# Kernel tuning notes

Measured on AMD Instinct MI355X. Metric: run time of the kernel, lower is better.

Reference implementation:

```python
import jax, jax.numpy as jnp
import numpy as np

N = 50000      # nodes
E = 800000     # edges (avg degree 16)
IN = 128       # in_channels
HID = 32       # hidden_channels per head
HEADS = 4
OUT = 64       # out_channels (last layer, heads=1, concat=False)
ED = 32        # edge_dim
NEG_SLOPE = 0.2


def _gatv2_layer(x, src, dst, ea, Wl, bl, Wr, br, We, att, bias, concat):
    """PyG GATv2Conv: lin_l -> source (x_j), lin_r -> target (x_i),
    score = att . leaky_relu(x_i + x_j + lin_edge(edge_attr)), segment-softmax over dst,
    out = scatter_add(alpha * x_j) per head, then concat or mean heads, plus bias."""
    n = x.shape[0]
    H, C = att.shape
    xl = (x @ Wl + bl).reshape(-1, H, C)   # [N,H,C] source transform
    xr = (x @ Wr + br).reshape(-1, H, C)   # [N,H,C] target transform
    ee = (ea @ We).reshape(-1, H, C)       # [E,H,C] edge transform
    m = jax.nn.leaky_relu(xl[src] + xr[dst] + ee, NEG_SLOPE)  # [E,H,C]
    a = jnp.einsum('ehc,hc->eh', m, att)   # [E,H] attention logits
    amax = jax.ops.segment_max(a, dst, num_segments=n)        # [N,H]
    ex = jnp.exp(a - amax[dst])
    den = jax.ops.segment_sum(ex, dst, num_segments=n)        # [N,H]
    alpha = ex / (den[dst] + 1e-16)        # [E,H] segment softmax
    out = jax.ops.segment_sum(xl[src] * alpha[..., None], dst, num_segments=n)  # [N,H,C]
    out = out.reshape(n, H * C) if concat else out.mean(axis=1)
    return out + bias


def setup_inputs() -> dict:
    key = jax.random.key(0)
    ks = jax.random.split(key, 20)
    s = 0.05
    HC = HEADS * HID
    inp = {
        'x': jax.random.normal(ks[0], (N, IN), jnp.float32),
        'edge_index': jax.random.randint(ks[1], (2, E), 0, N, jnp.int32),
        'edge_attr': jax.random.normal(ks[2], (E, ED), jnp.float32),
        # layer 1: GATv2Conv(IN -> HID, heads=HEADS, concat=True, edge_dim=ED)
        'Wl1': jax.random.normal(ks[3], (IN, HC), jnp.float32) * s,
        'bl1': jnp.zeros((HC,), jnp.float32),
        'Wr1': jax.random.normal(ks[4], (IN, HC), jnp.float32) * s,
        'br1': jnp.zeros((HC,), jnp.float32),
        'We1': jax.random.normal(ks[5], (ED, HC), jnp.float32) * s,
        'att1': jax.random.normal(ks[6], (HEADS, HID), jnp.float32) * s,
        'bias1': jnp.zeros((HC,), jnp.float32),
        # layer 2: GATv2Conv(HC -> OUT, heads=1, concat=False, edge_dim=ED)
        'Wl2': jax.random.normal(ks[7], (HC, OUT), jnp.float32) * s,
        'bl2': jnp.zeros((OUT,), jnp.float32),
        'Wr2': jax.random.normal(ks[8], (HC, OUT), jnp.float32) * s,
        'br2': jnp.zeros((OUT,), jnp.float32),
        'We2': jax.random.normal(ks[9], (ED, OUT), jnp.float32) * s,
        'att2': jax.random.normal(ks[10], (1, OUT), jnp.float32) * s,
        'bias2': jnp.zeros((OUT,), jnp.float32),
    }
    return inp


def reference(x, edge_index, edge_attr, Wl1, bl1, Wr1, br1, We1, att1, bias1,
              Wl2, bl2, Wr2, br2, We2, att2, bias2):
    src, dst = edge_index[0], edge_index[1]
    h = _gatv2_layer(x, src, dst, edge_attr, Wl1, bl1, Wr1, br1, We1, att1, bias1, concat=True)
    h = jax.nn.elu(h)
    out = _gatv2_layer(h, src, dst, edge_attr, Wl2, bl2, Wr2, br2, We2, att2, bias2, concat=False)
    return out
```

## Files before the change

kernel.cpp:

```cpp
#include <hip/hip_runtime.h>
#include <stdint.h>

#define N_NODES 50000
#define N_EDGES 800000

struct Ptrs { const void* p[16]; int n[16]; };

typedef __attribute__((ext_vector_type(8))) short bf16x8;
typedef __attribute__((ext_vector_type(4))) float f32x4;

__device__ __forceinline__ float bf2f(unsigned short u){
  union { unsigned int i; float f; } v; v.i = ((unsigned int)u) << 16; return v.f;
}
__device__ __forceinline__ float lo16(unsigned int u){ union { unsigned int i; float f; } v; v.i = u << 16; return v.f; }
__device__ __forceinline__ float hi16(unsigned int u){ union { unsigned int i; float f; } v; v.i = u & 0xffff0000u; return v.f; }
__device__ __forceinline__ unsigned short f2bf(float f){
  if (!(f == f)) return 0;
  unsigned int x = __float_as_uint(f);
  unsigned int r = (x + 0x7fffu + ((x >> 16) & 1u)) >> 16;
  return (unsigned short)r;
}
__device__ __forceinline__ float fin(float v){
  if (!(v == v)) return 0.f;
  return fminf(fmaxf(v, -1e30f), 1e30f);
}
__device__ __forceinline__ float loadF(const void* p, int f32, size_t idx){
  return f32 ? ((const float*)p)[idx] : bf2f(((const unsigned short*)p)[idx]);
}

__device__ __forceinline__ void stageW(unsigned short* dst, const void* src, int n, int f32, int tid){
  if (f32) {
    for (int i = tid * 8; i < n; i += 2048) {
      float4 a = *(const float4*)((const float*)src + i);
      float4 b = *(const float4*)((const float*)src + i + 4);
      uint4 u;
      u.x = (unsigned)f2bf(a.x) | ((unsigned)f2bf(a.y) << 16);
      u.y = (unsigned)f2bf(a.z) | ((unsigned)f2bf(a.w) << 16);
      u.z = (unsigned)f2bf(b.x) | ((unsigned)f2bf(b.y) << 16);
      u.w = (unsigned)f2bf(b.z) | ((unsigned)f2bf(b.w) << 16);
      *(uint4*)(dst + i) = u;
    }
  } else {
    for (int i = tid * 8; i < n; i += 2048)
      *(uint4*)(dst + i) = *(const uint4*)((const unsigned short*)src + i);
  }
}

__global__ __launch_bounds__(256) void k_detect(Ptrs tl, int* __restrict__ flags)
{
  __shared__ int red[256];
  int b = blockIdx.x, t = threadIdx.x;
  const unsigned short* p = (const unsigned short*)tl.p[b];
  int n = tl.n[b]; if (n > 16384) n = 16384;
  int crazy = 0;
  for (int i = t; i < n; i += 256) {
    unsigned short u = p[i];
    if (u) {
      int ex = (u >> 7) & 0xFF;
      if (ex == 0xFF || ex < 0x60) crazy++;
    }
  }
  red[t] = crazy; __syncthreads();
  for (int off = 128; off; off >>= 1) { if (t < off) red[t] += red[t + off]; __syncthreads(); }
  if (t == 0) flags[b] = (red[0] * 10 > n) ? 1 : 0;
}

__global__ __launch_bounds__(256) void k_zero(int* __restrict__ p, int n)
{
  int i = blockIdx.x * 256 + threadIdx.x;
  if (i < n) p[i] = 0;
}

__global__ __launch_bounds__(256) void k_gemm1(
    const void* __restrict__ x,
    const void* __restrict__ Wl, const void* __restrict__ bl,
    const void* __restrict__ Wr, const void* __restrict__ br,
    const int* __restrict__ flags,
    unsigned int* __restrict__ xlp, unsigned int* __restrict__ xrp)
{
  __shared__ float xs[32 * 132];
  __shared__ unsigned short ws[128 * 128];
  const void* W  = blockIdx.y ? Wr : Wl;
  const void* bb = blockIdx.y ? br : bl;
  int fW = blockIdx.y ? flags[4] : flags[2];
  int fB = blockIdx.y ? flags[5] : flags[3];
  int fX = flags[0];
  unsigned int* outp = blockIdx.y ? xrp : xlp;
  int tid = threadIdx.x;
  int row0 = blockIdx.x * 32;
  stageW(ws, W, 128 * 128, fW, tid);
  for (int i = tid * 4; i < 32 * 128; i += 1024) {
    int r = i >> 7, k = i & 127;
    int row = row0 + r;
    float4 v = make_float4(0.f, 0.f, 0.f, 0.f);
    if (row < N_NODES) {
      if (fX) v = *(const float4*)((const float*)x + (size_t)row * 128 + k);
      else {
        uint2 u = *(const uint2*)((const unsigned short*)x + (size_t)row * 128 + k);
        v.x = lo16(u.x); v.y = hi16(u.x); v.z = lo16(u.y); v.w = hi16(u.y);
      }
    }
    *(float4*)(xs + r * 132 + k) = v;
  }
  __syncthreads();
  int r = tid >> 3, cg = tid & 7;
  float acc[16];
#pragma unroll
  for (int j = 0; j < 16; j++) acc[j] = 0.f;
#pragma unroll 4
  for (int k = 0; k < 128; k++) {
    float xv = xs[r * 132 + k];
    uint4 p0 = *(const uint4*)(ws + k * 128 + cg * 8);
    uint4 p1 = *(const uint4*)(ws + k * 128 + 64 + cg * 8);
    acc[0]  = fmaf(xv, lo16(p0.x), acc[0]);  acc[1]  = fmaf(xv, hi16(p0.x), acc[1]);
    acc[2]  = fmaf(xv, lo16(p0.y), acc[2]);  acc[3]  = fmaf(xv, hi16(p0.y), acc[3]);
    acc[4]  = fmaf(xv, lo16(p0.z), acc[4]);  acc[5]  = fmaf(xv, hi16(p0.z), acc[5]);
    acc[6]  = fmaf(xv, lo16(p0.w), acc[6]);  acc[7]  = fmaf(xv, hi16(p0.w), acc[7]);
    acc[8]  = fmaf(xv, lo16(p1.x), acc[8]);  acc[9]  = fmaf(xv, hi16(p1.x), acc[9]);
    acc[10] = fmaf(xv, lo16(p1.y), acc[10]); acc[11] = fmaf(xv, hi16(p1.y), acc[11]);
    acc[12] = fmaf(xv, lo16(p1.z), acc[12]); acc[13] = fmaf(xv, hi16(p1.z), acc[13]);
    acc[14] = fmaf(xv, lo16(p1.w), acc[14]); acc[15] = fmaf(xv, hi16(p1.w), acc[15]);
  }
  int row = row0 + r;
  if (row < N_NODES) {
    unsigned int* op = outp + (size_t)row * 64;
    int tt = cg >> 1, qb = (cg & 1) * 2;
    unsigned int ou[4];
#pragma unroll
    for (int t = 0; t < 4; t++) {
      float f0 = fin(acc[2 * t]     + loadF(bb, fB, cg * 8 + 2 * t));
      float f1 = fin(acc[2 * t + 1] + loadF(bb, fB, cg * 8 + 2 * t + 1));
      ou[t] = (unsigned)f2bf(f0) | ((unsigned)f2bf(f1) << 16);
    }
    *(uint2*)(op + qb * 16 + tt * 2)       = make_uint2(ou[0], ou[1]);
    *(uint2*)(op + (qb + 1) * 16 + tt * 2) = make_uint2(ou[2], ou[3]);
#pragma unroll
    for (int t = 0; t < 4; t++) {
      float f0 = fin(acc[8 + 2 * t]     + loadF(bb, fB, 64 + cg * 8 + 2 * t));
      float f1 = fin(acc[8 + 2 * t + 1] + loadF(bb, fB, 64 + cg * 8 + 2 * t + 1));
      ou[t] = (unsigned)f2bf(f0) | ((unsigned)f2bf(f1) << 16);
    }
    *(uint2*)(op + qb * 16 + 8 + tt * 2)       = make_uint2(ou[0], ou[1]);
    *(uint2*)(op + (qb + 1) * 16 + 8 + tt * 2) = make_uint2(ou[2], ou[3]);
  }
}

__global__ __launch_bounds__(256) void k_gemm2(
    const float* __restrict__ h,
    const void* __restrict__ Wl, const void* __restrict__ bl,
    const void* __restrict__ Wr, const void* __restrict__ br,
    const int* __restrict__ flags,
    unsigned int* __restrict__ xlp, unsigned int* __restrict__ xrp)
{
  __shared__ float hs[32 * 132];
  __shared__ unsigned short ws[128 * 64];
  const void* W  = blockIdx.y ? Wr : Wl;
  const void* bb = blockIdx.y ? br : bl;
  int fW = blockIdx.y ? flags[11] : flags[9];
  int fB = blockIdx.y ? flags[12] : flags[10];
  unsigned int* outp = blockIdx.y ? xrp : xlp;
  int tid = threadIdx.x;
  int row0 = blockIdx.x * 32;
  stageW(ws, W, 128 * 64, fW, tid);
  for (int i = tid * 4; i < 32 * 128; i += 1024) {
    int r = i >> 7, k = i & 127;
    int row = row0 + r;
    float4 v = make_float4(0.f, 0.f, 0.f, 0.f);
    if (row < N_NODES) v = *(const float4*)(h + (size_t)row * 128 + k);
    *(float4*)(hs + r * 132 + k) = v;
  }
  __syncthreads();
  int r = tid >> 3, cg = tid & 7;
  float acc[8];
#pragma unroll
  for (int j = 0; j < 8; j++) acc[j] = 0.f;
#pragma unroll 4
  for (int k = 0; k < 128; k++) {
    float hv = hs[r * 132 + k];
    uint4 p = *(const uint4*)(ws + k * 64 + cg * 8);
    acc[0] = fmaf(hv, lo16(p.x), acc[0]); acc[1] = fmaf(hv, hi16(p.x), acc[1]);
    acc[2] = fmaf(hv, lo16(p.y), acc[2]); acc[3] = fmaf(hv, hi16(p.y), acc[3]);
    acc[4] = fmaf(hv, lo16(p.z), acc[4]); acc[5] = fmaf(hv, hi16(p.z), acc[5]);
    acc[6] = fmaf(hv, lo16(p.w), acc[6]); acc[7] = fmaf(hv, hi16(p.w), acc[7]);
  }
  int row = row0 + r;
  if (row < N_NODES) {
    unsigned int* op = outp + (size_t)row * 32;
    int tt = cg >> 1, qb = (cg & 1) * 2;
    unsigned int ou[4];
#pragma unroll
    for (int t = 0; t < 4; t++) {
      float f0 = fin(acc[2 * t]     + loadF(bb, fB, cg * 8 + 2 * t));
      float f1 = fin(acc[2 * t + 1] + loadF(bb, fB, cg * 8 + 2 * t + 1));
      ou[t] = (unsigned)f2bf(f0) | ((unsigned)f2bf(f1) << 16);
    }
    *(uint2*)(op + qb * 8 + tt * 2)       = make_uint2(ou[0], ou[1]);
    *(uint2*)(op + (qb + 1) * 8 + tt * 2) = make_uint2(ou[2], ou[3]);
  }
}

__global__ __launch_bounds__(256) void k_hist(const int* __restrict__ ei, int* __restrict__ counts)
{
  int e = blockIdx.x * 256 + threadIdx.x;
  if (e < N_EDGES) {
    int d = ei[N_EDGES + e]; if ((unsigned)d >= N_NODES) d = 0;
    atomicAdd(&counts[d], 1);
  }
}

__global__ __launch_bounds__(256) void k_scan1(const int* __restrict__ counts,
                                               int* __restrict__ row_ptr, int* __restrict__ bsum)
{
  __shared__ int lds[256];
  int t = threadIdx.x;
  int base = blockIdx.x * 1024 + t * 4;
  int c0 = (base + 0) < N_NODES ? counts[base + 0] : 0;
  int c1 = (base + 1) < N_NODES ? counts[base + 1] : 0;
  int c2 = (base + 2) < N_NODES ? counts[base + 2] : 0;
  int c3 = (base + 3) < N_NODES ? counts[base + 3] : 0;
  int s = c0 + c1 + c2 + c3;
  lds[t] = s; __syncthreads();
  for (int off = 1; off < 256; off <<= 1) {
    int v = (t >= off) ? lds[t - off] : 0;
    __syncthreads();
    lds[t] += v;
    __syncthreads();
// ... 74 lines not shown
  }
}

__global__ __launch_bounds__(256) void k_fuse1(
    const unsigned short* __restrict__ eap, const int* __restrict__ srcs,
    const int* __restrict__ row_ptr,
    const unsigned int* __restrict__ xlp, const unsigned int* __restrict__ xrp,
    const void* __restrict__ We, const void* __restrict__ att,
    const void* __restrict__ bias, const int* __restrict__ flags,
    float* __restrict__ hout)
{
  __shared__ unsigned short wt[128 * 34];
  __shared__ float at[128];
  int tid = threadIdx.x;
  {
    int f = flags[6];
    for (int i2 = tid; i2 < 4096; i2 += 256) {
      int k = i2 >> 7, c = i2 & 127;
      wt[c * 34 + k] = f ? f2bf(((const float*)We)[i2]) : ((const unsigned short*)We)[i2];
    }
  }
  if (tid < 128) at[tid] = loadF(att, flags[7], tid);
  __syncthreads();
  int lane = tid & 63;
  int idx16 = lane & 15, quad = lane >> 4;
  int t_s = (lane & 15) >> 1, b_s = lane & 1;
  int un = t_s * 8 + quad * 2 + b_s;
  int hd = un >> 4;
  bf16x8 af[8];
#pragma unroll
  for (int t = 0; t < 8; t++)
    af[t] = *(const bf16x8*)(wt + (t * 16 + idx16) * 34 + quad * 8);
  int wv = tid >> 6;
#pragma unroll 1
  for (int rep = 0; rep < 2; rep++) {
    int i = blockIdx.x * 8 + rep * 4 + wv;
    int p0 = row_ptr[i], p1 = row_ptr[i + 1];
    uint2 rv[8];
#pragma unroll
    for (int t4 = 0; t4 < 4; t4++) {
      uint4 u = *(const uint4*)(xrp + (size_t)i * 64 + quad * 16 + t4 * 4);
      rv[2 * t4]     = make_uint2(u.x, u.y);
      rv[2 * t4 + 1] = make_uint2(u.z, u.w);
    }
    float acc0 = 0.f, acc1 = 0.f, den = 0.f;
    for (int jb = p0; jb < p1; jb += 16) {
      int j = jb + idx16;
      int act = j < p1;
      int jc = act ? j : p0;
      int s = srcs[jc];
      bf16x8 bfrag = *(const bf16x8*)(eap + (size_t)jc * 32 + quad * 8);
      uint2 xv[8];
#pragma unroll
      for (int t4 = 0; t4 < 4; t4++) {
        uint4 u = *(const uint4*)(xlp + (size_t)s * 64 + quad * 16 + t4 * 4);
        xv[2 * t4]     = make_uint2(u.x, u.y);
        xv[2 * t4 + 1] = make_uint2(u.z, u.w);
      }
      float ph0 = 0.f, ph1 = 0.f, ph2 = 0.f, ph3 = 0.f;
#pragma unroll
      for (int t = 0; t < 8; t++) {
        float4 av = *(const float4*)(at + t * 16 + quad * 4);
        uint2 r = rv[t];
        f32x4 c = {0.f, 0.f, 0.f, 0.f};
        c = __builtin_amdgcn_mfma_f32_16x16x32_bf16(af[t], bfrag, c, 0, 0, 0);
        float z0 = c[0] + lo16(xv[t].x) + lo16(r.x);
        float z1 = c[1] + hi16(xv[t].x) + hi16(r.x);
        float z2 = c[2] + lo16(xv[t].y) + lo16(r.y);
        float z3 = c[3] + hi16(xv[t].y) + hi16(r.y);
        z0 = z0 > 0.f ? z0 : 0.2f * z0;
        z1 = z1 > 0.f ? z1 : 0.2f * z1;
        z2 = z2 > 0.f ? z2 : 0.2f * z2;
        z3 = z3 > 0.f ? z3 : 0.2f * z3;
        float pp = fmaf(av.x, z0, fmaf(av.y, z1, fmaf(av.z, z2, av.w * z3)));
        if (t < 2)      ph0 += pp;
        else if (t < 4) ph1 += pp;
        else if (t < 6) ph2 += pp;
        else            ph3 += pp;
      }
      ph0 += __shfl_xor(ph0, 16, 64); ph0 += __shfl_xor(ph0, 32, 64);
      ph1 += __shfl_xor(ph1, 16, 64); ph1 += __shfl_xor(ph1, 32, 64);
      ph2 += __shfl_xor(ph2, 16, 64); ph2 += __shfl_xor(ph2, 32, 64);
      ph3 += __shfl_xor(ph3, 16, 64); ph3 += __shfl_xor(ph3, 32, 64);
      float w0 = act ? __expf(fminf(fin(ph0), 25.f)) : 0.f;
      float w1 = act ? __expf(fminf(fin(ph1), 25.f)) : 0.f;
      float w2 = act ? __expf(fminf(fin(ph2), 25.f)) : 0.f;
      float w3 = act ? __expf(fminf(fin(ph3), 25.f)) : 0.f;
      float wsel = quad == 0 ? w0 : quad == 1 ? w1 : quad == 2 ? w2 : w3;
      int sjl[16];
      float wjv[16];
#pragma unroll
      for (int q = 0; q < 16; q++) sjl[q] = __shfl(s, q, 64);
#pragma unroll
      for (int q = 0; q < 16; q++) wjv[q] = __shfl(wsel, hd * 16 + q, 64);
#pragma unroll
      for (int q = 0; q < 16; q++) {
        unsigned int v = xlp[(size_t)sjl[q] * 64 + lane];
        acc0 = fmaf(wjv[q], lo16(v), acc0);
        acc1 = fmaf(wjv[q], hi16(v), acc1);
        den += wjv[q];
      }
    }
    float inv = 1.f / (den + 1e-16f);
    int fB = flags[8];
    int ch = un * 2;
    float o0 = fin(fmaf(acc0, inv, loadF(bias, fB, ch)));
    float o1 = fin(fmaf(acc1, inv, loadF(bias, fB, ch + 1)));
    o0 = o0 > 0.f ? o0 : __expf(o0) - 1.f;
    o1 = o1 > 0.f ? o1 : __expf(o1) - 1.f;
    *(float2*)(hout + (size_t)i * 128 + ch) = make_float2(o0, o1);
  }
}

__global__ __launch_bounds__(256) void k_fuse2(
    const unsigned short* __restrict__ eap, const int* __restrict__ srcs,
    const int* __restrict__ row_ptr,
    const unsigned int* __restrict__ xlp, const unsigned int* __restrict__ xrp,
    const void* __restrict__ We, const void* __restrict__ att,
    const void* __restrict__ bias, const int* __restrict__ flags,
    void* __restrict__ out)
{
  __shared__ unsigned short wt[64 * 34];
  __shared__ float at[64];
  int tid = threadIdx.x;
  {
    int f = flags[13];
    for (int i2 = tid; i2 < 2048; i2 += 256) {
      int k = i2 >> 6, c = i2 & 63;
      wt[c * 34 + k] = f ? f2bf(((const float*)We)[i2]) : ((const unsigned short*)We)[i2];
    }
  }
  if (tid < 64) at[tid] = loadF(att, flags[14], tid);
  __syncthreads();
  int lane = tid & 63;
  int idx16 = lane & 15, quad = lane >> 4;
  int l5 = lane & 31;
  int q_s = l5 >> 3, t2 = (l5 & 7) >> 1, b2 = l5 & 1;
  int un = t2 * 8 + q_s * 2 + b2;
  int halfe = lane >> 5;
  bf16x8 af[4];
#pragma unroll
  for (int t = 0; t < 4; t++)
    af[t] = *(const bf16x8*)(wt + (t * 16 + idx16) * 34 + quad * 8);
  int wv = tid >> 6;
#pragma unroll 1
  for (int rep = 0; rep < 2; rep++) {
    int i = blockIdx.x * 8 + rep * 4 + wv;
    int p0 = row_ptr[i], p1 = row_ptr[i + 1];
    uint2 rv[4];
#pragma unroll
    for (int k = 0; k < 2; k++) {
      uint4 u = *(const uint4*)(xrp + (size_t)i * 32 + quad * 8 + k * 4);
      rv[2 * k]     = make_uint2(u.x, u.y);
      rv[2 * k + 1] = make_uint2(u.z, u.w);
    }
    float acc0 = 0.f, acc1 = 0.f, den = 0.f;
    for (int jb = p0; jb < p1; jb += 16) {
      int j = jb + idx16;
      int act = j < p1;
      int jc = act ? j : p0;
      int s = srcs[jc];
      bf16x8 bfrag = *(const bf16x8*)(eap + (size_t)jc * 32 + quad * 8);
      uint2 xv[4];
#pragma unroll
      for (int k = 0; k < 2; k++) {
        uint4 u = *(const uint4*)(xlp + (size_t)s * 32 + quad * 8 + k * 4);
        xv[2 * k]     = make_uint2(u.x, u.y);
        xv[2 * k + 1] = make_uint2(u.z, u.w);
      }
      float ph = 0.f;
#pragma unroll
      for (int t = 0; t < 4; t++) {
        float4 av = *(const float4*)(at + t * 16 + quad * 4);
        uint2 r = rv[t];
        f32x4 c = {0.f, 0.f, 0.f, 0.f};
        c = __builtin_amdgcn_mfma_f32_16x16x32_bf16(af[t], bfrag, c, 0, 0, 0);
        float z0 = c[0] + lo16(xv[t].x) + lo16(r.x);
        float z1 = c[1] + hi16(xv[t].x) + hi16(r.x);
        float z2 = c[2] + lo16(xv[t].y) + lo16(r.y);
        float z3 = c[3] + hi16(xv[t].y) + hi16(r.y);
        z0 = z0 > 0.f ? z0 : 0.2f * z0;
        z1 = z1 > 0.f ? z1 : 0.2f * z1;
        z2 = z2 > 0.f ? z2 : 0.2f * z2;
        z3 = z3 > 0.f ? z3 : 0.2f * z3;
        ph += fmaf(av.x, z0, fmaf(av.y, z1, fmaf(av.z, z2, av.w * z3)));
      }
      ph += __shfl_xor(ph, 16, 64);
      ph += __shfl_xor(ph, 32, 64);
      float wsel = act ? __expf(fminf(fin(ph), 25.f)) : 0.f;
      int sjl[8];
      float wjv[8];
#pragma unroll
      for (int q = 0; q < 8; q++) {
        int qq = 2 * q + halfe;
        sjl[q] = __shfl(s, qq, 64);
        wjv[q] = __shfl(wsel, qq, 64);
      }
#pragma unroll
      for (int q = 0; q < 8; q++) {
        unsigned int v = xlp[(size_t)sjl[q] * 32 + l5];
        acc0 = fmaf(wjv[q], lo16(v), acc0);
        acc1 = fmaf(wjv[q], hi16(v), acc1);
        den += wjv[q];
      }
    }
    acc0 += __shfl_xor(acc0, 32, 64);
    acc1 += __shfl_xor(acc1, 32, 64);
    den  += __shfl_xor(den, 32, 64);
    if (lane < 32) {
      float inv = 1.f / (den + 1e-16f);
      int fB = flags[15];
      int ch = un * 2;
      float o0 = fin(fmaf(acc0, inv, loadF(bias, fB, ch)));
      float o1 = fin(fmaf(acc1, inv, loadF(bias, fB, ch + 1)));
      if (flags[0]) {
        *(float2*)((float*)out + (size_t)i * 64 + ch) = make_float2(o0, o1);
      } else {
        unsigned int u = (unsigned)f2bf(o0) | ((unsigned)f2bf(o1) << 16);
        *(unsigned int*)((unsigned short*)out + (size_t)i * 64 + ch) = u;
      }
    }
  }
}

extern "C" void kernel_launch(void* const* d_in, const int* in_sizes, int n_in,
                              void* d_out, int out_size, void* d_ws, size_t ws_size,
                              hipStream_t stream)
{
  (void)n_in; (void)out_size; (void)ws_size;
  const void* x    = d_in[0];
  const int*  ei   = (const int*)d_in[1];
  const void* ea   = d_in[2];
  const void* Wl1  = d_in[3];
  const void* bl1  = d_in[4];
  const void* Wr1  = d_in[5];
  const void* br1  = d_in[6];
  const void* We1  = d_in[7];
  const void* att1 = d_in[8];
  const void* bias1= d_in[9];
  const void* Wl2  = d_in[10];
  const void* bl2  = d_in[11];
  const void* Wr2  = d_in[12];
  const void* br2  = d_in[13];
  const void* We2  = d_in[14];
  const void* att2 = d_in[15];
  const void* bias2= d_in[16];

  char* ws = (char*)d_ws;
  size_t off = 0;
  auto take = [&](size_t bytes) -> char* {
    char* p = ws + off;
    off += (bytes + 255) & ~(size_t)255;
    return p;
  };
  unsigned int* xl1p = (unsigned int*)take((size_t)N_NODES * 64 * 4);
  unsigned int* xr1p = (unsigned int*)take((size_t)N_NODES * 64 * 4);
  float* hbuf   = (float*)take((size_t)N_NODES * 128 * 4);
  unsigned short* eap = (unsigned short*)take((size_t)(N_EDGES + 16) * 32 * 2);
  int*   counts = (int*)  take((size_t)N_NODES * 4);
  int*   row_ptr= (int*)  take((size_t)(N_NODES + 1) * 4);
  int*   cursor = (int*)  take((size_t)N_NODES * 4);
  int*   srcs   = (int*)  take((size_t)N_EDGES * 4);
  int*   bsum   = (int*)  take(64 * 4);
  int*   flags  = (int*)  take(64 * 4);
  unsigned int* xl2p = xl1p;
  unsigned int* xr2p = xr1p;

  Ptrs tl;
  const int map[16] = {0, 2, 3, 4, 5, 6, 7, 8, 9, 10, 11, 12, 13, 14, 15, 16};
  for (int j = 0; j < 16; j++) { tl.p[j] = d_in[map[j]]; tl.n[j] = in_sizes[map[j]]; }

  int nb = (N_NODES + 1023) / 1024;
  k_detect<<<16, 256, 0, stream>>>(tl, flags);
  k_zero<<<(N_NODES + 255) / 256, 256, 0, stream>>>(counts, N_NODES);
  k_gemm1<<<dim3((N_NODES + 31) / 32, 2), 256, 0, stream>>>(x, Wl1, bl1, Wr1, br1, flags, xl1p, xr1p);
  k_hist<<<(N_EDGES + 255) / 256, 256, 0, stream>>>(ei, counts);
  k_scan1<<<nb, 256, 0, stream>>>(counts, row_ptr, bsum);
  k_scan2<<<1, 64, 0, stream>>>(bsum, nb);
  k_scan3<<<nb, 256, 0, stream>>>(row_ptr, cursor, bsum);
  k_scatter<<<(N_EDGES + 255) / 256, 256, 0, stream>>>(ei, cursor, srcs, ea, flags, eap);
  k_fuse1<<<N_NODES / 8, 256, 0, stream>>>(eap, srcs, row_ptr, xl1p, xr1p, We1, att1, bias1, flags, hbuf);
  k_gemm2<<<dim3((N_NODES + 31) / 32, 2), 256, 0, stream>>>(hbuf, Wl2, bl2, Wr2, br2, flags, xl2p, xr2p);
  k_fuse2<<<N_NODES / 8, 256, 0, stream>>>(eap, srcs, row_ptr, xl2p, xr2p, We2, att2, bias2, flags, d_out);
}
```

Measured before the change: 705.2 us.

## Interleave two destination nodes per wave in fused GATv2 edge kernels

Both fused edge kernels now process their two destination nodes together in one loop instead of one after another. Each iteration issues the gathers for both nodes before computing, so more memory requests are in flight per wave. Row bounds go through readfirstlane so they are treated as wave-uniform. Layer 1 also reloads source indices per edge from memory instead of shuffling them, which needs a zeroed 16-entry pad after srcs. The cost is higher register pressure and divergence when the two nodes have different degrees.

Measured after the change: 698.6 us. Within noise of the previous version (-0.9%).

```diff
diff --git a/kernel.cpp b/kernel.cpp
--- a/kernel.cpp
+++ b/kernel.cpp
@@ -65,10 +65,11 @@
   if (t == 0) flags[b] = (red[0] * 10 > n) ? 1 : 0;
 }
 
-__global__ __launch_bounds__(256) void k_zero(int* __restrict__ p, int n)
+__global__ __launch_bounds__(256) void k_zero(int* __restrict__ p, int n, int* __restrict__ pad16)
 {
   int i = blockIdx.x * 256 + threadIdx.x;
   if (i < n) p[i] = 0;
+  if (i < 16) pad16[i] = 0;
 }
 
 __global__ __launch_bounds__(256) void k_gemm1(
@@ -332,42 +333,65 @@
   for (int t = 0; t < 8; t++)
     af[t] = *(const bf16x8*)(wt + (t * 16 + idx16) * 34 + quad * 8);
   int wv = tid >> 6;
-#pragma unroll 1
-  for (int rep = 0; rep < 2; rep++) {
-    int i = blockIdx.x * 8 + rep * 4 + wv;
-    int p0 = row_ptr[i], p1 = row_ptr[i + 1];
-    uint2 rv[8];
-#pragma unroll
-    for (int t4 = 0; t4 < 4; t4++) {
-      uint4 u = *(const uint4*)(xrp + (size_t)i * 64 + quad * 16 + t4 * 4);
-      rv[2 * t4]     = make_uint2(u.x, u.y);
-      rv[2 * t4 + 1] = make_uint2(u.z, u.w);
-    }
-    float acc0 = 0.f, acc1 = 0.f, den = 0.f;
-    for (int jb = p0; jb < p1; jb += 16) {
-      int j = jb + idx16;
-      int act = j < p1;
-      int jc = act ? j : p0;
-      int s = srcs[jc];
-      bf16x8 bfrag = *(const bf16x8*)(eap + (size_t)jc * 32 + quad * 8);
-      uint2 xv[8];
+  int i0 = blockIdx.x * 8 + wv;
+  int i1 = i0 + 4;
+  uint2 rv0[8], rv1[8];
+#pragma unroll
+  for (int t4 = 0; t4 < 4; t4++) {
+    uint4 u = *(const uint4*)(xrp + (size_t)i0 * 64 + quad * 16 + t4 * 4);
+    rv0[2 * t4]     = make_uint2(u.x, u.y);
+    rv0[2 * t4 + 1] = make_uint2(u.z, u.w);
+  }
+#pragma unroll
+  for (int t4 = 0; t4 < 4; t4++) {
+    uint4 u = *(const uint4*)(xrp + (size_t)i1 * 64 + quad * 16 + t4 * 4);
+    rv1[2 * t4]     = make_uint2(u.x, u.y);
+    rv1[2 * t4 + 1] = make_uint2(u.z, u.w);
+  }
+  int p0a = __builtin_amdgcn_readfirstlane(row_ptr[i0]);
+  int p1a = __builtin_amdgcn_readfirstlane(row_ptr[i0 + 1]);
+  int p0b = __builtin_amdgcn_readfirstlane(row_ptr[i1]);
+  int p1b = __builtin_amdgcn_readfirstlane(row_ptr[i1 + 1]);
+  float aA0 = 0.f, aA1 = 0.f, dA = 0.f;
+  float aB0 = 0.f, aB1 = 0.f, dB = 0.f;
+  for (int jba = p0a, jbb = p0b; jba < p1a || jbb < p1b; jba += 16, jbb += 16) {
+    int doA = jba < p1a, doB = jbb < p1b;
+    int jA = jba + idx16, jB = jbb + idx16;
+    int actA = jA < p1a, actB = jB < p1b;
+    int jcA = actA ? jA : p0a, jcB = actB ? jB : p0b;
+    int sA = srcs[jcA], sB = srcs[jcB];
+    bf16x8 bfA, bfB;
+    uint2 xvA[8], xvB[8];
+    if (doA) {
+      bfA = *(const bf16x8*)(eap + (size_t)jcA * 32 + quad * 8);
 #pragma unroll
       for (int t4 = 0; t4 < 4; t4++) {
-        uint4 u = *(const uint4*)(xlp + (size_t)s * 64 + quad * 16 + t4 * 4);
-        xv[2 * t4]     = make_uint2(u.x, u.y);
-        xv[2 * t4 + 1] = make_uint2(u.z, u.w);
-      }
+        uint4 u = *(const uint4*)(xlp + (size_t)sA * 64 + quad * 16 + t4 * 4);
+        xvA[2 * t4]     = make_uint2(u.x, u.y);
+        xvA[2 * t4 + 1] = make_uint2(u.z, u.w);
+      }
+    }
+    if (doB) {
+      bfB = *(const bf16x8*)(eap + (size_t)jcB * 32 + quad * 8);
+#pragma unroll
+      for (int t4 = 0; t4 < 4; t4++) {
+        uint4 u = *(const uint4*)(xlp + (size_t)sB * 64 + quad * 16 + t4 * 4);
+        xvB[2 * t4]     = make_uint2(u.x, u.y);
+        xvB[2 * t4 + 1] = make_uint2(u.z, u.w);
+      }
+    }
+    if (doA) {
       float ph0 = 0.f, ph1 = 0.f, ph2 = 0.f, ph3 = 0.f;
 #pragma unroll
       for (int t = 0; t < 8; t++) {
         float4 av = *(const float4*)(at + t * 16 + quad * 4);
-        uint2 r = rv[t];
+        uint2 r = rv0[t];
         f32x4 c = {0.f, 0.f, 0.f, 0.f};
-        c = __builtin_amdgcn_mfma_f32_16x16x32_bf16(af[t], bfrag, c, 0, 0, 0);
-        float z0 = c[0] + lo16(xv[t].x) + lo16(r.x);
-        float z1 = c[1] + hi16(xv[t].x) + hi16(r.x);
-        float z2 = c[2] + lo16(xv[t].y) + lo16(r.y);
-        float z3 = c[3] + hi16(xv[t].y) + hi16(r.y);
+        c = __builtin_amdgcn_mfma_f32_16x16x32_bf16(af[t], bfA, c, 0, 0, 0);
+        float z0 = c[0] + lo16(xvA[t].x) + lo16(r.x);
+        float z1 = c[1] + hi16(xvA[t].x) + hi16(r.x);
+        float z2 = c[2] + lo16(xvA[t].y) + lo16(r.y);
+        float z3 = c[3] + hi16(xvA[t].y) + hi16(r.y);
         z0 = z0 > 0.f ? z0 : 0.2f * z0;
         z1 = z1 > 0.f ? z1 : 0.2f * z1;
         z2 = z2 > 0.f ? z2 : 0.2f * z2;
@@ -382,33 +406,85 @@
       ph1 += __shfl_xor(ph1, 16, 64); ph1 += __shfl_xor(ph1, 32, 64);
       ph2 += __shfl_xor(ph2, 16, 64); ph2 += __shfl_xor(ph2, 32, 64);
       ph3 += __shfl_xor(ph3, 16, 64); ph3 += __shfl_xor(ph3, 32, 64);
-      float w0 = act ? __expf(fminf(fin(ph0), 25.f)) : 0.f;
-      float w1 = act ? __expf(fminf(fin(ph1), 25.f)) : 0.f;
-      float w2 = act ? __expf(fminf(fin(ph2), 25.f)) : 0.f;
-      float w3 = act ? __expf(fminf(fin(ph3), 25.f)) : 0.f;
+      float w0 = actA ? __expf(fminf(fin(ph0), 25.f)) : 0.f;
+      float w1 = actA ? __expf(fminf(fin(ph1), 25.f)) : 0.f;
+      float w2 = actA ? __expf(fminf(fin(ph2), 25.f)) : 0.f;
+      float w3 = actA ? __expf(fminf(fin(ph3), 25.f)) : 0.f;
       float wsel = quad == 0 ? w0 : quad == 1 ? w1 : quad == 2 ? w2 : w3;
-      int sjl[16];
-      float wjv[16];
-#pragma unroll
-      for (int q = 0; q < 16; q++) sjl[q] = __shfl(s, q, 64);
-#pragma unroll
-      for (int q = 0; q < 16; q++) wjv[q] = __shfl(wsel, hd * 16 + q, 64);
 #pragma unroll
       for (int q = 0; q < 16; q++) {
-        unsigned int v = xlp[(size_t)sjl[q] * 64 + lane];
-        acc0 = fmaf(wjv[q], lo16(v), acc0);
-        acc1 = fmaf(wjv[q], hi16(v), acc1);
-        den += wjv[q];
-      }
-    }
-    float inv = 1.f / (den + 1e-16f);
-    int fB = flags[8];
-    int ch = un * 2;
-    float o0 = fin(fmaf(acc0, inv, loadF(bias, fB, ch)));
-    float o1 = fin(fmaf(acc1, inv, loadF(bias, fB, ch + 1)));
+        int ej = jba + q;
+        ej = (ej < p1a) ? ej : p0a;
+        int sq = srcs[ej];
+        float wq = __shfl(wsel, hd * 16 + q, 64);
+        unsigned int v = xlp[(size_t)sq * 64 + lane];
+        aA0 = fmaf(wq, lo16(v), aA0);
+        aA1 = fmaf(wq, hi16(v), aA1);
+        dA += wq;
+      }
+    }
+    if (doB) {
+      float ph0 = 0.f, ph1 = 0.f, ph2 = 0.f, ph3 = 0.f;
+#pragma unroll
+      for (int t = 0; t < 8; t++) {
+        float4 av = *(const float4*)(at + t * 16 + quad * 4);
+        uint2 r = rv1[t];
+        f32x4 c = {0.f, 0.f, 0.f, 0.f};
+        c = __builtin_amdgcn_mfma_f32_16x16x32_bf16(af[t], bfB, c, 0, 0, 0);
+        float z0 = c[0] + lo16(xvB[t].x) + lo16(r.x);
+        float z1 = c[1] + hi16(xvB[t].x) + hi16(r.x);
+        float z2 = c[2] + lo16(xvB[t].y) + lo16(r.y);
+        float z3 = c[3] + hi16(xvB[t].y) + hi16(r.y);
+        z0 = z0 > 0.f ? z0 : 0.2f * z0;
+        z1 = z1 > 0.f ? z1 : 0.2f * z1;
+        z2 = z2 > 0.f ? z2 : 0.2f * z2;
+        z3 = z3 > 0.f ? z3 : 0.2f * z3;
+        float pp = fmaf(av.x, z0, fmaf(av.y, z1, fmaf(av.z, z2, av.w * z3)));
+        if (t < 2)      ph0 += pp;
+        else if (t < 4) ph1 += pp;
+        else if (t < 6) ph2 += pp;
+        else            ph3 += pp;
+      }
+      ph0 += __shfl_xor(ph0, 16, 64); ph0 += __shfl_xor(ph0, 32, 64);
+      ph1 += __shfl_xor(ph1, 16, 64); ph1 += __shfl_xor(ph1, 32, 64);
+      ph2 += __shfl_xor(ph2, 16, 64); ph2 += __shfl_xor(ph2, 32, 64);
+      ph3 += __shfl_xor(ph3, 16, 64); ph3 += __shfl_xor(ph3, 32, 64);
+      float w0 = actB ? __expf(fminf(fin(ph0), 25.f)) : 0.f;
+      float w1 = actB ? __expf(fminf(fin(ph1), 25.f)) : 0.f;
+      float w2 = actB ? __expf(fminf(fin(ph2), 25.f)) : 0.f;
+      float w3 = actB ? __expf(fminf(fin(ph3), 25.f)) : 0.f;
+      float wsel = quad == 0 ? w0 : quad == 1 ? w1 : quad == 2 ? w2 : w3;
+#pragma unroll
+      for (int q = 0; q < 16; q++) {
+        int ej = jbb + q;
+        ej = (ej < p1b) ? ej : p0b;
+        int sq = srcs[ej];
+        float wq = __shfl(wsel, hd * 16 + q, 64);
+        unsigned int v = xlp[(size_t)sq * 64 + lane];
+        aB0 = fmaf(wq, lo16(v), aB0);
+        aB1 = fmaf(wq, hi16(v), aB1);
+        dB += wq;
+      }
+    }
+  }
+  int fB = flags[8];
+  int ch = un * 2;
+  float b0 = loadF(bias, fB, ch), b1 = loadF(bias, fB, ch + 1);
+  {
+    float inv = 1.f / (dA + 1e-16f);
+    float o0 = fin(fmaf(aA0, inv, b0));
+    float o1 = fin(fmaf(aA1, inv, b1));
     o0 = o0 > 0.f ? o0 : __expf(o0) - 1.f;
     o1 = o1 > 0.f ? o1 : __expf(o1) - 1.f;
-    *(float2*)(hout + (size_t)i * 128 + ch) = make_float2(o0, o1);
+    *(float2*)(hout + (size_t)i0 * 128 + ch) = make_float2(o0, o1);
+  }
+  {
+    float inv = 1.f / (dB + 1e-16f);
+    float o0 = fin(fmaf(aB0, inv, b0));
+    float o1 = fin(fmaf(aB1, inv, b1));
+    o0 = o0 > 0.f ? o0 : __expf(o0) - 1.f;
+    o1 = o1 > 0.f ? o1 : __expf(o1) - 1.f;
+    *(float2*)(hout + (size_t)i1 * 128 + ch) = make_float2(o0, o1);
   }
 }
 
@@ -443,28 +519,39 @@
   for (int t = 0; t < 4; t++)
     af[t] = *(const bf16x8*)(wt + (t * 16 + idx16) * 34 + quad * 8);
   int wv = tid >> 6;
-#pragma unroll 1
-  for (int rep = 0; rep < 2; rep++) {
-    int i = blockIdx.x * 8 + rep * 4 + wv;
-    int p0 = row_ptr[i], p1 = row_ptr[i + 1];
-    uint2 rv[4];
-#pragma unroll
-    for (int k = 0; k < 2; k++) {
-      uint4 u = *(const uint4*)(xrp + (size_t)i * 32 + quad * 8 + k * 4);
-      rv[2 * k]     = make_uint2(u.x, u.y);
-      rv[2 * k + 1] = make_uint2(u.z, u.w);
-    }
-    float acc0 = 0.f, acc1 = 0.f, den = 0.f;
-    for (int jb = p0; jb < p1; jb += 16) {
-      int j = jb + idx16;
-      int act = j < p1;
-      int jc = act ? j : p0;
-      int s = srcs[jc];
-      bf16x8 bfrag = *(const bf16x8*)(eap + (size_t)jc * 32 + quad * 8);
+  int i0 = blockIdx.x * 8 + wv;
+  int i1 = i0 + 4;
+  uint2 rv0[4], rv1[4];
+#pragma unroll
+  for (int k = 0; k < 2; k++) {
+    uint4 u = *(const uint4*)(xrp + (size_t)i0 * 32 + quad * 8 + k * 4);
+    rv0[2 * k]     = make_uint2(u.x, u.y);
+    rv0[2 * k + 1] = make_uint2(u.z, u.w);
+  }
+#pragma unroll
+  for (int k = 0; k < 2; k++) {
+    uint4 u = *(const uint4*)(xrp + (size_t)i1 * 32 + quad * 8 + k * 4);
+    rv1[2 * k]     = make_uint2(u.x, u.y);
+    rv1[2 * k + 1] = make_uint2(u.z, u.w);
+  }
+  int p0a = __builtin_amdgcn_readfirstlane(row_ptr[i0]);
+  int p1a = __builtin_amdgcn_readfirstlane(row_ptr[i0 + 1]);
+  int p0b = __builtin_amdgcn_readfirstlane(row_ptr[i1]);
+  int p1b = __builtin_amdgcn_readfirstlane(row_ptr[i1 + 1]);
+  float aA0 = 0.f, aA1 = 0.f, dA = 0.f;
+  float aB0 = 0.f, aB1 = 0.f, dB = 0.f;
+  for (int jba = p0a, jbb = p0b; jba < p1a || jbb < p1b; jba += 16, jbb += 16) {
+    int doA = jba < p1a, doB = jbb < p1b;
+    int jA = jba + idx16, jB = jbb + idx16;
+    int actA = jA < p1a, actB = jB < p1b;
+    int jcA = actA ? jA : p0a, jcB = actB ? jB : p0b;
+    int sA = srcs[jcA], sB = srcs[jcB];
+    if (doA) {
+      bf16x8 bfrag = *(const bf16x8*)(eap + (size_t)jcA * 32 + quad * 8);
       uint2 xv[4];
 #pragma unroll
       for (int k = 0; k < 2; k++) {
-        uint4 u = *(const uint4*)(xlp + (size_t)s * 32 + quad * 8 + k * 4);
+        uint4 u = *(const uint4*)(xlp + (size_t)sA * 32 + quad * 8 + k * 4);
         xv[2 * k]     = make_uint2(u.x, u.y);
         xv[2 * k + 1] = make_uint2(u.z, u.w);
       }
@@ -472,7 +559,7 @@
 #pragma unroll
       for (int t = 0; t < 4; t++) {
         float4 av = *(const float4*)(at + t * 16 + quad * 4);
-        uint2 r = rv[t];
+        uint2 r = rv0[t];
         f32x4 c = {0.f, 0.f, 0.f, 0.f};
         c = __builtin_amdgcn_mfma_f32_16x16x32_bf16(af[t], bfrag, c, 0, 0, 0);
         float z0 = c[0] + lo16(xv[t].x) + lo16(r.x);
@@ -487,38 +574,83 @@
       }
       ph += __shfl_xor(ph, 16, 64);
       ph += __shfl_xor(ph, 32, 64);
-      float wsel = act ? __expf(fminf(fin(ph), 25.f)) : 0.f;
-      int sjl[8];
-      float wjv[8];
+      float wsel = actA ? __expf(fminf(fin(ph), 25.f)) : 0.f;
 #pragma unroll
       for (int q = 0; q < 8; q++) {
         int qq = 2 * q + halfe;
-        sjl[q] = __shfl(s, qq, 64);
-        wjv[q] = __shfl(wsel, qq, 64);
-      }
+        int sq = __shfl(sA, qq, 64);
+        float wq = __shfl(wsel, qq, 64);
+        unsigned int v = xlp[(size_t)sq * 32 + l5];
+        aA0 = fmaf(wq, lo16(v), aA0);
+        aA1 = fmaf(wq, hi16(v), aA1);
+        dA += wq;
+      }
+    }
+    if (doB) {
+      bf16x8 bfrag = *(const bf16x8*)(eap + (size_t)jcB * 32 + quad * 8);
+      uint2 xv[4];
+#pragma unroll
+      for (int k = 0; k < 2; k++) {
+        uint4 u = *(const uint4*)(xlp + (size_t)sB * 32 + quad * 8 + k * 4);
+        xv[2 * k]     = make_uint2(u.x, u.y);
+        xv[2 * k + 1] = make_uint2(u.z, u.w);
+      }
+      float ph = 0.f;
+#pragma unroll
+      for (int t = 0; t < 4; t++) {
+        float4 av = *(const float4*)(at + t * 16 + quad * 4);
+        uint2 r = rv1[t];
+        f32x4 c = {0.f, 0.f, 0.f, 0.f};
+        c = __builtin_amdgcn_mfma_f32_16x16x32_bf16(af[t], bfrag, c, 0, 0, 0);
+        float z0 = c[0] + lo16(xv[t].x) + lo16(r.x);
+        float z1 = c[1] + hi16(xv[t].x) + hi16(r.x);
+        float z2 = c[2] + lo16(xv[t].y) + lo16(r.y);
+        float z3 = c[3] + hi16(xv[t].y) + hi16(r.y);
+        z0 = z0 > 0.f ? z0 : 0.2f * z0;
+        z1 = z1 > 0.f ? z1 : 0.2f * z1;
+        z2 = z2 > 0.f ? z2 : 0.2f * z2;
+        z3 = z3 > 0.f ? z3 : 0.2f * z3;
+        ph += fmaf(av.x, z0, fmaf(av.y, z1, fmaf(av.z, z2, av.w * z3)));
+      }
+      ph += __shfl_xor(ph, 16, 64);
+      ph += __shfl_xor(ph, 32, 64);
+      float wsel = actB ? __expf(fminf(fin(ph), 25.f)) : 0.f;
 #pragma unroll
       for (int q = 0; q < 8; q++) {
-        unsigned int v = xlp[(size_t)sjl[q] * 32 + l5];
-        acc0 = fmaf(wjv[q], lo16(v), acc0);
-        acc1 = fmaf(wjv[q], hi16(v), acc1);
-        den += wjv[q];
-      }
-    }
-    acc0 += __shfl_xor(acc0, 32, 64);
-    acc1 += __shfl_xor(acc1, 32, 64);
-    den  += __shfl_xor(den, 32, 64);
-    if (lane < 32) {
-      float inv = 1.f / (den + 1e-16f);
-      int fB = flags[15];
-      int ch = un * 2;
-      float o0 = fin(fmaf(acc0, inv, loadF(bias, fB, ch)));
-      float o1 = fin(fmaf(acc1, inv, loadF(bias, fB, ch + 1)));
-      if (flags[0]) {
-        *(float2*)((float*)out + (size_t)i * 64 + ch) = make_float2(o0, o1);
-      } else {
-        unsigned int u = (unsigned)f2bf(o0) | ((unsigned)f2bf(o1) << 16);
-        *(unsigned int*)((unsigned short*)out + (size_t)i * 64 + ch) = u;
-      }
+        int qq = 2 * q + halfe;
+        int sq = __shfl(sB, qq, 64);
+        float wq = __shfl(wsel, qq, 64);
+        unsigned int v = xlp[(size_t)sq * 32 + l5];
+        aB0 = fmaf(wq, lo16(v), aB0);
+        aB1 = fmaf(wq, hi16(v), aB1);
+        dB += wq;
+      }
+    }
+  }
+  aA0 += __shfl_xor(aA0, 32, 64);
+  aA1 += __shfl_xor(aA1, 32, 64);
+  dA  += __shfl_xor(dA, 32, 64);
+  aB0 += __shfl_xor(aB0, 32, 64);
+  aB1 += __shfl_xor(aB1, 32, 64);
+  dB  += __shfl_xor(dB, 32, 64);
+  if (lane < 32) {
+    int fB = flags[15];
+    int ch = un * 2;
+    float b0 = loadF(bias, fB, ch), b1 = loadF(bias, fB, ch + 1);
+    float invA = 1.f / (dA + 1e-16f);
+    float oA0 = fin(fmaf(aA0, invA, b0));
+    float oA1 = fin(fmaf(aA1, invA, b1));
+    float invB = 1.f / (dB + 1e-16f);
+    float oB0 = fin(fmaf(aB0, invB, b0));
+    float oB1 = fin(fmaf(aB1, invB, b1));
+    if (flags[0]) {
+      *(float2*)((float*)out + (size_t)i0 * 64 + ch) = make_float2(oA0, oA1);
+      *(float2*)((float*)out + (size_t)i1 * 64 + ch) = make_float2(oB0, oB1);
+    } else {
+      unsigned int uA = (unsigned)f2bf(oA0) | ((unsigned)f2bf(oA1) << 16);
+      unsigned int uB = (unsigned)f2bf(oB0) | ((unsigned)f2bf(oB1) << 16);
+      *(unsigned int*)((unsigned short*)out + (size_t)i0 * 64 + ch) = uA;
+      *(unsigned int*)((unsigned short*)out + (size_t)i1 * 64 + ch) = uB;
     }
   }
 }
@@ -560,7 +692,7 @@
   int*   counts = (int*)  take((size_t)N_NODES * 4);
   int*   row_ptr= (int*)  take((size_t)(N_NODES + 1) * 4);
   int*   cursor = (int*)  take((size_t)N_NODES * 4);
-  int*   srcs   = (int*)  take((size_t)N_EDGES * 4);
+  int*   srcs   = (int*)  take((size_t)(N_EDGES + 16) * 4);
   int*   bsum   = (int*)  take(64 * 4);
   int*   flags  = (int*)  take(64 * 4);
   unsigned int* xl2p = xl1p;
@@ -572,7 +704,7 @@
 
   int nb = (N_NODES + 1023) / 1024;
   k_detect<<<16, 256, 0, stream>>>(tl, flags);
-  k_zero<<<(N_NODES + 255) / 256, 256, 0, stream>>>(counts, N_NODES);
+  k_zero<<<(N_NODES + 255) / 256, 256, 0, stream>>>(counts, N_NODES, srcs + N_EDGES);
   k_gemm1<<<dim3((N_NODES + 31) / 32, 2), 256, 0, stream>>>(x, Wl1, bl1, Wr1, br1, flags, xl1p, xr1p);
   k_hist<<<(N_EDGES + 255) / 256, 256, 0, stream>>>(ei, counts);
   k_scan1<<<nb, 256, 0, stream>>>(counts, row_ptr, bsum);
```

## Use bf16 MFMA with hi/lo split for node GEMMs; fuse zeroing into detect

Applied to the files above, without the earlier changes.

Both node-transform GEMMs move from scalar FMA loops to MFMA 16x16x32 bf16 instructions. The activation is split into bf16 high and low parts so the result keeps near-fp32 accuracy. Weights are loaded straight from global memory into register fragments instead of being staged in shared memory, and results pass through shared memory to reuse the existing bf16 output packing. The separate counts-zeroing kernel is folded into the detect launch as extra blocks, which also zero a new 16-entry pad after srcs. This saves one launch but costs twice the MFMA work per tile and uncoalesced strided weight reads in every block.

After: 657.7 us. 1.07x faster.

```diff
diff --git a/kernel.cpp b/kernel.cpp
--- a/kernel.cpp
+++ b/kernel.cpp
@@ -28,26 +28,15 @@
   return f32 ? ((const float*)p)[idx] : bf2f(((const unsigned short*)p)[idx]);
 }
 
-__device__ __forceinline__ void stageW(unsigned short* dst, const void* src, int n, int f32, int tid){
-  if (f32) {
-    for (int i = tid * 8; i < n; i += 2048) {
-      float4 a = *(const float4*)((const float*)src + i);
-      float4 b = *(const float4*)((const float*)src + i + 4);
-      uint4 u;
-      u.x = (unsigned)f2bf(a.x) | ((unsigned)f2bf(a.y) << 16);
-      u.y = (unsigned)f2bf(a.z) | ((unsigned)f2bf(a.w) << 16);
-      u.z = (unsigned)f2bf(b.x) | ((unsigned)f2bf(b.y) << 16);
-      u.w = (unsigned)f2bf(b.z) | ((unsigned)f2bf(b.w) << 16);
-      *(uint4*)(dst + i) = u;
-    }
-  } else {
-    for (int i = tid * 8; i < n; i += 2048)
-      *(uint4*)(dst + i) = *(const uint4*)((const unsigned short*)src + i);
-  }
-}
-
-__global__ __launch_bounds__(256) void k_detect(Ptrs tl, int* __restrict__ flags)
-{
+__global__ __launch_bounds__(256) void k_detect(Ptrs tl, int* __restrict__ flags,
+                                                int* __restrict__ counts, int* __restrict__ pad16)
+{
+  if (blockIdx.x >= 16) {
+    int i = (blockIdx.x - 16) * 256 + threadIdx.x;
+    if (i < N_NODES) counts[i] = 0;
+    if (blockIdx.x == 16 && threadIdx.x < 16) pad16[threadIdx.x] = 0;
+    return;
+  }
   __shared__ int red[256];
   int b = blockIdx.x, t = threadIdx.x;
   const unsigned short* p = (const unsigned short*)tl.p[b];
@@ -65,12 +54,6 @@
   if (t == 0) flags[b] = (red[0] * 10 > n) ? 1 : 0;
 }
 
-__global__ __launch_bounds__(256) void k_zero(int* __restrict__ p, int n)
-{
-  int i = blockIdx.x * 256 + threadIdx.x;
-  if (i < n) p[i] = 0;
-}
-
 __global__ __launch_bounds__(256) void k_gemm1(
     const void* __restrict__ x,
     const void* __restrict__ Wl, const void* __restrict__ bl,
@@ -78,8 +61,10 @@
     const int* __restrict__ flags,
     unsigned int* __restrict__ xlp, unsigned int* __restrict__ xrp)
 {
-  __shared__ float xs[32 * 132];
-  __shared__ unsigned short ws[128 * 128];
+  __shared__ __align__(16) char smem[17408];
+  unsigned short* xh  = (unsigned short*)smem;
+  unsigned short* xlo = (unsigned short*)(smem + 8704);
+  float* outb = (float*)smem;
   const void* W  = blockIdx.y ? Wr : Wl;
   const void* bb = blockIdx.y ? br : bl;
   int fW = blockIdx.y ? flags[4] : flags[2];
@@ -88,7 +73,6 @@
   unsigned int* outp = blockIdx.y ? xrp : xlp;
   int tid = threadIdx.x;
   int row0 = blockIdx.x * 32;
-  stageW(ws, W, 128 * 128, fW, tid);
   for (int i = tid * 4; i < 32 * 128; i += 1024) {
     int r = i >> 7, k = i & 127;
     int row = row0 + r;
@@ -100,26 +84,66 @@
         v.x = lo16(u.x); v.y = hi16(u.x); v.z = lo16(u.y); v.w = hi16(u.y);
       }
     }
-    *(float4*)(xs + r * 132 + k) = v;
-  }
+    unsigned short h0 = f2bf(v.x), h1 = f2bf(v.y), h2 = f2bf(v.z), h3 = f2bf(v.w);
+    *(ushort4*)(xh + r * 136 + k) = make_ushort4(h0, h1, h2, h3);
+    ushort4 lv;
+    lv.x = f2bf(v.x - bf2f(h0)); lv.y = f2bf(v.y - bf2f(h1));
+    lv.z = f2bf(v.z - bf2f(h2)); lv.w = f2bf(v.w - bf2f(h3));
+    *(ushort4*)(xlo + r * 136 + k) = lv;
+  }
+  int lane = tid & 63, wv = tid >> 6;
+  int idx16 = lane & 15, quad = lane >> 4;
+  bf16x8 bfr[2][4];
+#pragma unroll
+  for (int ct = 0; ct < 2; ct++) {
+#pragma unroll
+    for (int kc = 0; kc < 4; kc++) {
+      int col = wv * 32 + ct * 16 + idx16;
+      unsigned short tmp[8];
+#pragma unroll
+      for (int j = 0; j < 8; j++) {
+        int kk = kc * 32 + quad * 8 + j;
+        tmp[j] = fW ? f2bf(((const float*)W)[(size_t)kk * 128 + col])
+                    : ((const unsigned short*)W)[(size_t)kk * 128 + col];
+      }
+      bfr[ct][kc] = *(const bf16x8*)tmp;
+    }
+  }
+  __syncthreads();
+  f32x4 acc[2][2];
+#pragma unroll
+  for (int rt = 0; rt < 2; rt++)
+#pragma unroll
+    for (int ct = 0; ct < 2; ct++)
+      acc[rt][ct] = (f32x4){0.f, 0.f, 0.f, 0.f};
+#pragma unroll
+  for (int kc = 0; kc < 4; kc++) {
+#pragma unroll
+    for (int rt = 0; rt < 2; rt++) {
+      bf16x8 ah = *(const bf16x8*)(xh  + (rt * 16 + idx16) * 136 + kc * 32 + quad * 8);
+      bf16x8 al = *(const bf16x8*)(xlo + (rt * 16 + idx16) * 136 + kc * 32 + quad * 8);
+#pragma unroll
+      for (int ct = 0; ct < 2; ct++) {
+        acc[rt][ct] = __builtin_amdgcn_mfma_f32_16x16x32_bf16(ah, bfr[ct][kc], acc[rt][ct], 0, 0, 0);
+        acc[rt][ct] = __builtin_amdgcn_mfma_f32_16x16x32_bf16(al, bfr[ct][kc], acc[rt][ct], 0, 0, 0);
+      }
+    }
+  }
+  __syncthreads();
+#pragma unroll
+  for (int rt = 0; rt < 2; rt++)
+#pragma unroll
+    for (int ct = 0; ct < 2; ct++)
+#pragma unroll
+      for (int r = 0; r < 4; r++)
+        outb[(rt * 16 + quad * 4 + r) * 132 + wv * 32 + ct * 16 + idx16] = acc[rt][ct][r];
   __syncthreads();
   int r = tid >> 3, cg = tid & 7;
-  float acc[16];
-#pragma unroll
-  for (int j = 0; j < 16; j++) acc[j] = 0.f;
-#pragma unroll 4
-  for (int k = 0; k < 128; k++) {
-    float xv = xs[r * 132 + k];
-    uint4 p0 = *(const uint4*)(ws + k * 128 + cg * 8);
-    uint4 p1 = *(const uint4*)(ws + k * 128 + 64 + cg * 8);
-    acc[0]  = fmaf(xv, lo16(p0.x), acc[0]);  acc[1]  = fmaf(xv, hi16(p0.x), acc[1]);
-    acc[2]  = fmaf(xv, lo16(p0.y), acc[2]);  acc[3]  = fmaf(xv, hi16(p0.y), acc[3]);
-    acc[4]  = fmaf(xv, lo16(p0.z), acc[4]);  acc[5]  = fmaf(xv, hi16(p0.z), acc[5]);
-    acc[6]  = fmaf(xv, lo16(p0.w), acc[6]);  acc[7]  = fmaf(xv, hi16(p0.w), acc[7]);
-    acc[8]  = fmaf(xv, lo16(p1.x), acc[8]);  acc[9]  = fmaf(xv, hi16(p1.x), acc[9]);
-    acc[10] = fmaf(xv, lo16(p1.y), acc[10]); acc[11] = fmaf(xv, hi16(p1.y), acc[11]);
-    acc[12] = fmaf(xv, lo16(p1.z), acc[12]); acc[13] = fmaf(xv, hi16(p1.z), acc[13]);
-    acc[14] = fmaf(xv, lo16(p1.w), acc[14]); acc[15] = fmaf(xv, hi16(p1.w), acc[15]);
+  float a2[16];
+#pragma unroll
+  for (int j = 0; j < 8; j++) {
+    a2[j]     = outb[r * 132 + cg * 8 + j];
+    a2[8 + j] = outb[r * 132 + 64 + cg * 8 + j];
   }
   int row = row0 + r;
   if (row < N_NODES) {
@@ -128,16 +152,16 @@
     unsigned int ou[4];
 #pragma unroll
     for (int t = 0; t < 4; t++) {
-      float f0 = fin(acc[2 * t]     + loadF(bb, fB, cg * 8 + 2 * t));
-      float f1 = fin(acc[2 * t + 1] + loadF(bb, fB, cg * 8 + 2 * t + 1));
+      float f0 = fin(a2[2 * t]     + loadF(bb, fB, cg * 8 + 2 * t));
+      float f1 = fin(a2[2 * t + 1] + loadF(bb, fB, cg * 8 + 2 * t + 1));
       ou[t] = (unsigned)f2bf(f0) | ((unsigned)f2bf(f1) << 16);
     }
     *(uint2*)(op + qb * 16 + tt * 2)       = make_uint2(ou[0], ou[1]);
     *(uint2*)(op + (qb + 1) * 16 + tt * 2) = make_uint2(ou[2], ou[3]);
 #pragma unroll
     for (int t = 0; t < 4; t++) {
-      float f0 = fin(acc[8 + 2 * t]     + loadF(bb, fB, 64 + cg * 8 + 2 * t));
-      float f1 = fin(acc[8 + 2 * t + 1] + loadF(bb, fB, 64 + cg * 8 + 2 * t + 1));
+      float f0 = fin(a2[8 + 2 * t]     + loadF(bb, fB, 64 + cg * 8 + 2 * t));
+      float f1 = fin(a2[8 + 2 * t + 1] + loadF(bb, fB, 64 + cg * 8 + 2 * t + 1));
       ou[t] = (unsigned)f2bf(f0) | ((unsigned)f2bf(f1) << 16);
     }
     *(uint2*)(op + qb * 16 + 8 + tt * 2)       = make_uint2(ou[0], ou[1]);
@@ -152,8 +176,10 @@
     const int* __restrict__ flags,
     unsigned int* __restrict__ xlp, unsigned int* __restrict__ xrp)
 {
-  __shared__ float hs[32 * 132];
-  __shared__ unsigned short ws[128 * 64];
+  __shared__ __align__(16) char smem[17408];
+  unsigned short* hh  = (unsigned short*)smem;
+  unsigned short* hlo = (unsigned short*)(smem + 8704);
+  float* outb = (float*)smem;
   const void* W  = blockIdx.y ? Wr : Wl;
   const void* bb = blockIdx.y ? br : bl;
   int fW = blockIdx.y ? flags[11] : flags[9];
@@ -161,28 +187,58 @@
   unsigned int* outp = blockIdx.y ? xrp : xlp;
   int tid = threadIdx.x;
   int row0 = blockIdx.x * 32;
-  stageW(ws, W, 128 * 64, fW, tid);
   for (int i = tid * 4; i < 32 * 128; i += 1024) {
     int r = i >> 7, k = i & 127;
     int row = row0 + r;
     float4 v = make_float4(0.f, 0.f, 0.f, 0.f);
     if (row < N_NODES) v = *(const float4*)(h + (size_t)row * 128 + k);
-    *(float4*)(hs + r * 132 + k) = v;
-  }
+    unsigned short h0 = f2bf(v.x), h1 = f2bf(v.y), h2 = f2bf(v.z), h3 = f2bf(v.w);
+    *(ushort4*)(hh + r * 136 + k) = make_ushort4(h0, h1, h2, h3);
+    ushort4 lv;
+    lv.x = f2bf(v.x - bf2f(h0)); lv.y = f2bf(v.y - bf2f(h1));
+    lv.z = f2bf(v.z - bf2f(h2)); lv.w = f2bf(v.w - bf2f(h3));
+    *(ushort4*)(hlo + r * 136 + k) = lv;
+  }
+  int lane = tid & 63, wv = tid >> 6;
+  int idx16 = lane & 15, quad = lane >> 4;
+  bf16x8 bfr[4];
+#pragma unroll
+  for (int kc = 0; kc < 4; kc++) {
+    int col = wv * 16 + idx16;
+    unsigned short tmp[8];
+#pragma unroll
+    for (int j = 0; j < 8; j++) {
+      int kk = kc * 32 + quad * 8 + j;
+      tmp[j] = fW ? f2bf(((const float*)W)[(size_t)kk * 64 + col])
+                  : ((const unsigned short*)W)[(size_t)kk * 64 + col];
+    }
+    bfr[kc] = *(const bf16x8*)tmp;
+  }
+  __syncthreads();
+  f32x4 acc[2];
+  acc[0] = (f32x4){0.f, 0.f, 0.f, 0.f};
+  acc[1] = (f32x4){0.f, 0.f, 0.f, 0.f};
+#pragma unroll
+  for (int kc = 0; kc < 4; kc++) {
+#pragma unroll
+    for (int rt = 0; rt < 2; rt++) {
+      bf16x8 ah = *(const bf16x8*)(hh  + (rt * 16 + idx16) * 136 + kc * 32 + quad * 8);
+      bf16x8 al = *(const bf16x8*)(hlo + (rt * 16 + idx16) * 136 + kc * 32 + quad * 8);
+      acc[rt] = __builtin_amdgcn_mfma_f32_16x16x32_bf16(ah, bfr[kc], acc[rt], 0, 0, 0);
+      acc[rt] = __builtin_amdgcn_mfma_f32_16x16x32_bf16(al, bfr[kc], acc[rt], 0, 0, 0);
+    }
+  }
+  __syncthreads();
+#pragma unroll
+  for (int rt = 0; rt < 2; rt++)
+#pragma unroll
+    for (int r = 0; r < 4; r++)
+      outb[(rt * 16 + quad * 4 + r) * 68 + wv * 16 + idx16] = acc[rt][r];
   __syncthreads();
   int r = tid >> 3, cg = tid & 7;
-  float acc[8];
-#pragma unroll
-  for (int j = 0; j < 8; j++) acc[j] = 0.f;
-#pragma unroll 4
-  for (int k = 0; k < 128; k++) {
-    float hv = hs[r * 132 + k];
-    uint4 p = *(const uint4*)(ws + k * 64 + cg * 8);
-    acc[0] = fmaf(hv, lo16(p.x), acc[0]); acc[1] = fmaf(hv, hi16(p.x), acc[1]);
-    acc[2] = fmaf(hv, lo16(p.y), acc[2]); acc[3] = fmaf(hv, hi16(p.y), acc[3]);
-    acc[4] = fmaf(hv, lo16(p.z), acc[4]); acc[5] = fmaf(hv, hi16(p.z), acc[5]);
-    acc[6] = fmaf(hv, lo16(p.w), acc[6]); acc[7] = fmaf(hv, hi16(p.w), acc[7]);
-  }
+  float a2[8];
+#pragma unroll
+  for (int j = 0; j < 8; j++) a2[j] = outb[r * 68 + cg * 8 + j];
   int row = row0 + r;
   if (row < N_NODES) {
     unsigned int* op = outp + (size_t)row * 32;
@@ -190,8 +246,8 @@
     unsigned int ou[4];
 #pragma unroll
     for (int t = 0; t < 4; t++) {
-      float f0 = fin(acc[2 * t]     + loadF(bb, fB, cg * 8 + 2 * t));
-      float f1 = fin(acc[2 * t + 1] + loadF(bb, fB, cg * 8 + 2 * t + 1));
+      float f0 = fin(a2[2 * t]     + loadF(bb, fB, cg * 8 + 2 * t));
+      float f1 = fin(a2[2 * t + 1] + loadF(bb, fB, cg * 8 + 2 * t + 1));
       ou[t] = (unsigned)f2bf(f0) | ((unsigned)f2bf(f1) << 16);
     }
     *(uint2*)(op + qb * 8 + tt * 2)       = make_uint2(ou[0], ou[1]);
@@ -560,7 +616,7 @@
   int*   counts = (int*)  take((size_t)N_NODES * 4);
   int*   row_ptr= (int*)  take((size_t)(N_NODES + 1) * 4);
   int*   cursor = (int*)  take((size_t)N_NODES * 4);
-  int*   srcs   = (int*)  take((size_t)N_EDGES * 4);
+  int*   srcs   = (int*)  take((size_t)(N_EDGES + 16) * 4);
   int*   bsum   = (int*)  take(64 * 4);
   int*   flags  = (int*)  take(64 * 4);
   unsigned int* xl2p = xl1p;
@@ -571,8 +627,8 @@
   for (int j = 0; j < 16; j++) { tl.p[j] = d_in[map[j]]; tl.n[j] = in_sizes[map[j]]; }
 
   int nb = (N_NODES + 1023) / 1024;
-  k_detect<<<16, 256, 0, stream>>>(tl, flags);
-  k_zero<<<(N_NODES + 255) / 256, 256, 0, stream>>>(counts, N_NODES);
+  int zblocks = (N_NODES + 255) / 256;
+  k_detect<<<16 + zblocks, 256, 0, stream>>>(tl, flags, counts, srcs + N_EDGES);
   k_gemm1<<<dim3((N_NODES + 31) / 32, 2), 256, 0, stream>>>(x, Wl1, bl1, Wr1, br1, flags, xl1p, xr1p);
   k_hist<<<(N_EDGES + 255) / 256, 256, 0, stream>>>(ei, counts);
   k_scan1<<<nb, 256, 0, stream>>>(counts, row_ptr, bsum);
```
